# Optimization experiments

Hardware: AMD Instinct MI355X
Metric: run time of the kernel (lower is better)

The kernel has to match this reference:

```python
import jax, jax.numpy as jnp
import numpy as np

N_NODES = 50000
N_EDGES = 1600000
IN_FEAT = 48
OUT_FEAT = 48
NUM_RELS = 8


def setup_inputs() -> dict:
    key = jax.random.key(0)
    ks = jax.random.split(key, 9)
    # xavier-ish scale for relu gain
    s1 = float(np.sqrt(2.0) * np.sqrt(6.0 / (IN_FEAT + IN_FEAT)))
    s2 = float(np.sqrt(2.0) * np.sqrt(6.0 / (IN_FEAT + OUT_FEAT)))
    return {
        "inputs": jax.random.normal(ks[0], (N_NODES, IN_FEAT), dtype=jnp.float32),
        "norm": jax.random.uniform(ks[1], (N_EDGES, 1), dtype=jnp.float32),
        "weight1": jax.random.uniform(ks[2], (NUM_RELS, IN_FEAT, IN_FEAT), jnp.float32, -s1, s1),
        "weight2": jax.random.uniform(ks[3], (NUM_RELS, IN_FEAT, OUT_FEAT), jnp.float32, -s2, s2),
        "bias1": jax.random.normal(ks[4], (IN_FEAT,), dtype=jnp.float32) * 0.1,
        "bias2": jax.random.normal(ks[5], (OUT_FEAT,), dtype=jnp.float32) * 0.1,
        "src": jax.random.randint(ks[6], (N_EDGES,), 0, N_NODES, dtype=jnp.int64) if jax.config.jax_enable_x64 else jax.random.randint(ks[6], (N_EDGES,), 0, N_NODES).astype(jnp.int32),
        "dst": jax.random.randint(ks[7], (N_EDGES,), 0, N_NODES).astype(jnp.int32),
        "rel_type": jax.random.randint(ks[8], (N_EDGES,), 0, NUM_RELS).astype(jnp.int32),
    }


def reference(inputs, norm, weight1, weight2, bias1, bias2, src, dst, rel_type):
    # Message depends only on (src node, relation): precompute per (node, rel).
    # Stage 1: h1[n,r,:] = relu(h[n] @ W1[r] + b1)   -> [N, R, in]
    h1 = jax.nn.relu(jnp.einsum('ni,rij->nrj', inputs, weight1) + bias1)
    # Stage 2: h2[n,r,:] = h1[n,r] @ W2[r]           -> [N, R, out]
    h2 = jnp.einsum('nrj,rjo->nro', h1, weight2)
    # Per-edge gather + norm scaling                 -> [E, out]
    msg = h2[src, rel_type] * norm
    # Scatter-sum aggregation to destination nodes   -> [N, out]
    agg = jax.ops.segment_sum(msg, dst, num_segments=inputs.shape[0])
    # apply_func: bias2 + activation
    return jax.nn.relu(agg + bias2)
```

## Files before the change

### kernel.cpp

```cpp
#include <hip/hip_runtime.h>

#define NN 50000
#define EE 1600000
#define FF 48
#define RR 8
#define H2_ROW 64
#define LSTR 72
#define CAP 96

#define XB 3125
#define WB 8
#define ZB 49
#define K1GRID (XB + WB + ZB)

#define H2TILES 391
#define H2BLKS (H2TILES * RR)
#define K2GRID (H2BLKS * 3)

typedef __attribute__((ext_vector_type(8))) short frag8;
typedef __attribute__((ext_vector_type(4))) float frag4f;

__device__ inline unsigned short bf16r(float f) {
    unsigned u = __float_as_uint(f);
    return (unsigned short)((u + 0x7FFFu + ((u >> 16) & 1u)) >> 16);
}
__device__ inline unsigned bf16pack2(float a, float b) {
    return (unsigned)bf16r(a) | ((unsigned)bf16r(b) << 16);
}

__global__ __launch_bounds__(256) void pre_kernel(
    const float* __restrict__ X, const float* __restrict__ W1,
    const float* __restrict__ W2, unsigned short* __restrict__ Xb,
    unsigned short* __restrict__ W1t, unsigned short* __restrict__ W2t,
    int* __restrict__ count)
{
    int b = blockIdx.x;
    if (b < XB) {
        int g = b * 256 + threadIdx.x;
        int seg = g & 15;
        uint2 v = make_uint2(0u, 0u);
        if (seg < 12) {
            float4 x = ((const float4*)X)[(size_t)(g >> 4) * 12 + seg];
            v = make_uint2(bf16pack2(x.x, x.y), bf16pack2(x.z, x.w));
        }
        ((uint2*)Xb)[g] = v;
        return;
    }
    if (b < XB + WB) {
        int r = b - XB;
        const float* w1 = W1 + (size_t)r * FF * FF;
        const float* w2 = W2 + (size_t)r * FF * FF;
        for (int idx = threadIdx.x; idx < 48 * 64; idx += 256) {
            int j = idx >> 6, k = idx & 63;
            W1t[(size_t)r * 48 * 64 + idx] = (k < FF) ? bf16r(w1[k * FF + j]) : (unsigned short)0;
            W2t[(size_t)r * 48 * 64 + idx] = (k < FF) ? bf16r(w2[k * FF + j]) : (unsigned short)0;
        }
        return;
    }
    int z = (b - XB - WB) * 256 + threadIdx.x;
    if (z < 12500) ((int4*)count)[z] = make_int4(0, 0, 0, 0);
}

__global__ __launch_bounds__(256) void h2_place_kernel(
    const unsigned short* __restrict__ Xb, const unsigned short* __restrict__ W1t,
    const unsigned short* __restrict__ W2t, const float* __restrict__ B1,
    const int* __restrict__ srcv, const int* __restrict__ dstv,
    const int* __restrict__ relv, const float* __restrict__ norm,
    int* __restrict__ count, unsigned* __restrict__ payload,
    unsigned short* __restrict__ H2)
{
    __shared__ unsigned short h1s[128 * LSTR];
    int b = blockIdx.x;
    int bmod = b - (b / 3) * 3;
    if (bmod != 0) {
        int p = (b / 3) * 2 + bmod - 1;
        int e = p * 256 + threadIdx.x;
        if (e < EE) {
            int d = dstv[e];
            int pos = atomicAdd(&count[d], 1);
            unsigned qn = (unsigned)(norm[e] * 8192.0f + 0.5f);
            if (qn > 8191u) qn = 8191u;
            unsigned rec = ((unsigned)(srcv[e] * 8 + relv[e]) << 13) | qn;
            if ((unsigned)pos < (unsigned)CAP)
                __builtin_nontemporal_store(rec, &payload[(size_t)d * CAP + pos]);
        }
        return;
    }
    int h    = b / 3;
    int r    = h & 7;
    int tile = h >> 3;
    int tid  = threadIdx.x;
    int w    = tid >> 6, ln = tid & 63, q = ln >> 4, lq = ln & 15;
    int nb   = tile * 128 + w * 32;

    unsigned short* myh1 = &h1s[(w * 32) * LSTR];
    for (int i = ln; i < 32 * 12; i += 64) {
        int rr = i / 12, cs = i - rr * 12;
        *(unsigned*)&myh1[rr * LSTR + 48 + cs * 2] = 0;
    }

    int row0 = nb + lq;      if (row0 >= NN) row0 = NN - 1;
    int row1 = nb + 16 + lq; if (row1 >= NN) row1 = NN - 1;
    const frag8 a00 = *(const frag8*)&Xb[(size_t)row0 * 64 + q * 8];
    const frag8 a01 = *(const frag8*)&Xb[(size_t)row0 * 64 + 32 + q * 8];
    const frag8 a10 = *(const frag8*)&Xb[(size_t)row1 * 64 + q * 8];
    const frag8 a11 = *(const frag8*)&Xb[(size_t)row1 * 64 + 32 + q * 8];

    const unsigned short* w1r = W1t + (size_t)r * 48 * 64;
    const unsigned short* w2r = W2t + (size_t)r * 48 * 64;

    #pragma unroll
    for (int t = 0; t < 3; ++t) {
        int col = t * 16 + lq;
        frag8 b0 = *(const frag8*)&w1r[(col << 6) + q * 8];
        frag8 b1 = *(const frag8*)&w1r[(col << 6) + 32 + q * 8];
        float bc = B1[col];
        frag4f acc0 = {bc, bc, bc, bc};
        frag4f acc1 = {bc, bc, bc, bc};
        acc0 = __builtin_amdgcn_mfma_f32_16x16x32_bf16(a00, b0, acc0, 0, 0, 0);
        acc0 = __builtin_amdgcn_mfma_f32_16x16x32_bf16(a01, b1, acc0, 0, 0, 0);
        acc1 = __builtin_amdgcn_mfma_f32_16x16x32_bf16(a10, b0, acc1, 0, 0, 0);
        acc1 = __builtin_amdgcn_mfma_f32_16x16x32_bf16(a11, b1, acc1, 0, 0, 0);
        #pragma unroll
        for (int g = 0; g < 4; ++g) {
            myh1[(q * 4 + g) * LSTR + col]      = bf16r(fmaxf(acc0[g], 0.0f));
            myh1[(16 + q * 4 + g) * LSTR + col] = bf16r(fmaxf(acc1[g], 0.0f));
        }
    }

    const frag8 c00 = *(const frag8*)&myh1[lq * LSTR + q * 8];
    const frag8 c01 = *(const frag8*)&myh1[lq * LSTR + 32 + q * 8];
    const frag8 c10 = *(const frag8*)&myh1[(16 + lq) * LSTR + q * 8];
    const frag8 c11 = *(const frag8*)&myh1[(16 + lq) * LSTR + 32 + q * 8];

    #pragma unroll
    for (int t = 0; t < 3; ++t) {
        int col = t * 16 + lq;
        frag8 b0 = *(const frag8*)&w2r[(col << 6) + q * 8];
        frag8 b1 = *(const frag8*)&w2r[(col << 6) + 32 + q * 8];
        frag4f acc0 = {0.f, 0.f, 0.f, 0.f};
        frag4f acc1 = {0.f, 0.f, 0.f, 0.f};
        acc0 = __builtin_amdgcn_mfma_f32_16x16x32_bf16(c00, b0, acc0, 0, 0, 0);
        acc0 = __builtin_amdgcn_mfma_f32_16x16x32_bf16(c01, b1, acc0, 0, 0, 0);
        acc1 = __builtin_amdgcn_mfma_f32_16x16x32_bf16(c10, b0, acc1, 0, 0, 0);
        acc1 = __builtin_amdgcn_mfma_f32_16x16x32_bf16(c11, b1, acc1, 0, 0, 0);
        #pragma unroll
        for (int g = 0; g < 4; ++g) {
            int n0 = nb + q * 4 + g;
            int n1 = nb + 16 + q * 4 + g;
            if (n0 < NN) H2[((size_t)n0 * RR + r) * H2_ROW + col] = bf16r(acc0[g]);
            if (n1 < NN) H2[((size_t)n1 * RR + r) * H2_ROW + col] = bf16r(acc1[g]);
        }
    }
}

__global__ __launch_bounds__(256) void gather_kernel(
    const unsigned short* __restrict__ H2, const unsigned* __restrict__ payload,
    const int* __restrict__ count, const float* __restrict__ B2,
    float* __restrict__ out)
{
    unsigned tid = blockIdx.x * 256u + threadIdx.x;
    unsigned n = tid / 12u;
    unsigned c = tid - n * 12u;
    if (n >= NN) return;

    int cnt = count[n];
    if (cnt > CAP) cnt = CAP;
    if (cnt < 0) cnt = 0;
    const unsigned* pl = payload + (size_t)n * CAP;
    float a0 = 0.f, a1 = 0.f, a2 = 0.f, a3 = 0.f;

    int e = 0;
    for (; e + 8 <= cnt; e += 8) {
        unsigned p[8];
        #pragma unroll
        for (int k = 0; k < 8; ++k) p[k] = pl[e + k];
        uint2 v[8];
        #pragma unroll
        for (int k = 0; k < 8; ++k)
            v[k] = ((const uint2*)(H2 + (size_t)(p[k] >> 13) * H2_ROW))[c];
        #pragma unroll
        for (int k = 0; k < 8; ++k) {
            float nm = (float)(p[k] & 8191u) * (1.0f / 8192.0f);
            a0 = fmaf(__uint_as_float(v[k].x << 16),         nm, a0);
            a1 = fmaf(__uint_as_float(v[k].x & 0xFFFF0000u), nm, a1);
            a2 = fmaf(__uint_as_float(v[k].y << 16),         nm, a2);
            a3 = fmaf(__uint_as_float(v[k].y & 0xFFFF0000u), nm, a3);
        }
    }
    for (; e < cnt; ++e) {
        unsigned p = pl[e];
        float nm = (float)(p & 8191u) * (1.0f / 8192.0f);
        uint2 v = ((const uint2*)(H2 + (size_t)(p >> 13) * H2_ROW))[c];
        a0 = fmaf(__uint_as_float(v.x << 16),         nm, a0);
        a1 = fmaf(__uint_as_float(v.x & 0xFFFF0000u), nm, a1);
        a2 = fmaf(__uint_as_float(v.y << 16),         nm, a2);
        a3 = fmaf(__uint_as_float(v.y & 0xFFFF0000u), nm, a3);
    }
    float4 b = ((const float4*)B2)[c];
    ((float4*)out)[(size_t)n * 12u + c] = make_float4(
        fmaxf(a0 + b.x, 0.f), fmaxf(a1 + b.y, 0.f),
        fmaxf(a2 + b.z, 0.f), fmaxf(a3 + b.w, 0.f));
}

extern "C" void kernel_launch(void* const* d_in, const int* in_sizes, int n_in,
                              void* d_out, int out_size, void* d_ws, size_t ws_size,
                              hipStream_t stream) {
    const float* X   = (const float*)d_in[0];
    const float* nrm = (const float*)d_in[1];
    const float* W1  = (const float*)d_in[2];
    const float* W2  = (const float*)d_in[3];
    const float* B1  = (const float*)d_in[4];
    const float* B2  = (const float*)d_in[5];
    const int*   src = (const int*)d_in[6];
    const int*   dst = (const int*)d_in[7];
    const int*   rel = (const int*)d_in[8];
    float* out = (float*)d_out;

    unsigned short* H2      = (unsigned short*)d_ws;
    unsigned*       payload = (unsigned*)(H2 + (size_t)NN * RR * H2_ROW);
    unsigned short* Xb      = (unsigned short*)(payload + (size_t)NN * CAP);
    unsigned short* W1t     = Xb + (size_t)NN * 64;
    unsigned short* W2t     = W1t + RR * 48 * 64;
    int*            count   = (int*)(W2t + RR * 48 * 64);

    pre_kernel<<<K1GRID, 256, 0, stream>>>(X, W1, W2, Xb, W1t, W2t, count);

    h2_place_kernel<<<K2GRID, 256, 0, stream>>>(
        Xb, W1t, W2t, B1, src, dst, rel, nrm, count, payload, H2);

    unsigned total = (unsigned)NN * 12u;
    gather_kernel<<<(total + 255) / 256, 256, 0, stream>>>(
        H2, payload, count, B2, out);
}
```

Baseline: 230.0 us.

## Fuse input bf16 conversion into h2 kernel, memset counts, unroll gather by 16

```diff
diff --git a/kernel.cpp b/kernel.cpp
--- a/kernel.cpp
+++ b/kernel.cpp
@@ -8,10 +8,7 @@
 #define LSTR 72
 #define CAP 96
 
-#define XB 3125
 #define WB 8
-#define ZB 49
-#define K1GRID (XB + WB + ZB)
 
 #define H2TILES 391
 #define H2BLKS (H2TILES * RR)
@@ -27,42 +24,29 @@
 __device__ inline unsigned bf16pack2(float a, float b) {
     return (unsigned)bf16r(a) | ((unsigned)bf16r(b) << 16);
 }
+__device__ inline frag8 pack8(float4 a, float4 b) {
+    union { frag8 f; unsigned u[4]; } r;
+    r.u[0] = bf16pack2(a.x, a.y); r.u[1] = bf16pack2(a.z, a.w);
+    r.u[2] = bf16pack2(b.x, b.y); r.u[3] = bf16pack2(b.z, b.w);
+    return r.f;
+}
 
 __global__ __launch_bounds__(256) void pre_kernel(
-    const float* __restrict__ X, const float* __restrict__ W1,
-    const float* __restrict__ W2, unsigned short* __restrict__ Xb,
-    unsigned short* __restrict__ W1t, unsigned short* __restrict__ W2t,
-    int* __restrict__ count)
+    const float* __restrict__ W1, const float* __restrict__ W2,
+    unsigned short* __restrict__ W1t, unsigned short* __restrict__ W2t)
 {
-    int b = blockIdx.x;
-    if (b < XB) {
-        int g = b * 256 + threadIdx.x;
-        int seg = g & 15;
-        uint2 v = make_uint2(0u, 0u);
-        if (seg < 12) {
-            float4 x = ((const float4*)X)[(size_t)(g >> 4) * 12 + seg];
-            v = make_uint2(bf16pack2(x.x, x.y), bf16pack2(x.z, x.w));
-        }
-        ((uint2*)Xb)[g] = v;
-        return;
-    }
-    if (b < XB + WB) {
-        int r = b - XB;
-        const float* w1 = W1 + (size_t)r * FF * FF;
-        const float* w2 = W2 + (size_t)r * FF * FF;
-        for (int idx = threadIdx.x; idx < 48 * 64; idx += 256) {
-            int j = idx >> 6, k = idx & 63;
-            W1t[(size_t)r * 48 * 64 + idx] = (k < FF) ? bf16r(w1[k * FF + j]) : (unsigned short)0;
-            W2t[(size_t)r * 48 * 64 + idx] = (k < FF) ? bf16r(w2[k * FF + j]) : (unsigned short)0;
-        }
-        return;
-    }
-    int z = (b - XB - WB) * 256 + threadIdx.x;
-    if (z < 12500) ((int4*)count)[z] = make_int4(0, 0, 0, 0);
+    int r = blockIdx.x;
+    const float* w1 = W1 + (size_t)r * FF * FF;
+    const float* w2 = W2 + (size_t)r * FF * FF;
+    for (int idx = threadIdx.x; idx < 48 * 64; idx += 256) {
+        int j = idx >> 6, k = idx & 63;
+        W1t[(size_t)r * 48 * 64 + idx] = (k < FF) ? bf16r(w1[k * FF + j]) : (unsigned short)0;
+        W2t[(size_t)r * 48 * 64 + idx] = (k < FF) ? bf16r(w2[k * FF + j]) : (unsigned short)0;
+    }
 }
 
 __global__ __launch_bounds__(256) void h2_place_kernel(
-    const unsigned short* __restrict__ Xb, const unsigned short* __restrict__ W1t,
+    const float* __restrict__ X, const unsigned short* __restrict__ W1t,
     const unsigned short* __restrict__ W2t, const float* __restrict__ B1,
     const int* __restrict__ srcv, const int* __restrict__ dstv,
     const int* __restrict__ relv, const float* __restrict__ norm,
@@ -101,10 +85,17 @@
 
     int row0 = nb + lq;      if (row0 >= NN) row0 = NN - 1;
     int row1 = nb + 16 + lq; if (row1 >= NN) row1 = NN - 1;
-    const frag8 a00 = *(const frag8*)&Xb[(size_t)row0 * 64 + q * 8];
-    const frag8 a01 = *(const frag8*)&Xb[(size_t)row0 * 64 + 32 + q * 8];
-    const frag8 a10 = *(const frag8*)&Xb[(size_t)row1 * 64 + q * 8];
-    const frag8 a11 = *(const frag8*)&Xb[(size_t)row1 * 64 + 32 + q * 8];
+    const float* x0 = X + (size_t)row0 * FF;
+    const float* x1 = X + (size_t)row1 * FF;
+
+    frag8 a00 = pack8(*(const float4*)(x0 + q * 8), *(const float4*)(x0 + q * 8 + 4));
+    frag8 a10 = pack8(*(const float4*)(x1 + q * 8), *(const float4*)(x1 + q * 8 + 4));
+    frag8 a01 = {0, 0, 0, 0, 0, 0, 0, 0};
+    frag8 a11 = {0, 0, 0, 0, 0, 0, 0, 0};
+    if (q < 2) {
+        a01 = pack8(*(const float4*)(x0 + 32 + q * 8), *(const float4*)(x0 + 36 + q * 8));
+        a11 = pack8(*(const float4*)(x1 + 32 + q * 8), *(const float4*)(x1 + 36 + q * 8));
+    }
 
     const unsigned short* w1r = W1t + (size_t)r * 48 * 64;
     const unsigned short* w2r = W2t + (size_t)r * 48 * 64;
@@ -171,6 +162,23 @@
     float a0 = 0.f, a1 = 0.f, a2 = 0.f, a3 = 0.f;
 
     int e = 0;
+    for (; e + 16 <= cnt; e += 16) {
+        unsigned p[16];
+        #pragma unroll
+        for (int k = 0; k < 16; ++k) p[k] = pl[e + k];
+        uint2 v[16];
+        #pragma unroll
+        for (int k = 0; k < 16; ++k)
+            v[k] = ((const uint2*)(H2 + (size_t)(p[k] >> 13) * H2_ROW))[c];
+        #pragma unroll
+        for (int k = 0; k < 16; ++k) {
+            float nm = (float)(p[k] & 8191u) * (1.0f / 8192.0f);
+            a0 = fmaf(__uint_as_float(v[k].x << 16),         nm, a0);
+            a1 = fmaf(__uint_as_float(v[k].x & 0xFFFF0000u), nm, a1);
+            a2 = fmaf(__uint_as_float(v[k].y << 16),         nm, a2);
+            a3 = fmaf(__uint_as_float(v[k].y & 0xFFFF0000u), nm, a3);
+        }
+    }
     for (; e + 8 <= cnt; e += 8) {
         unsigned p[8];
         #pragma unroll
@@ -219,15 +227,16 @@
 
     unsigned short* H2      = (unsigned short*)d_ws;
     unsigned*       payload = (unsigned*)(H2 + (size_t)NN * RR * H2_ROW);
-    unsigned short* Xb      = (unsigned short*)(payload + (size_t)NN * CAP);
-    unsigned short* W1t     = Xb + (size_t)NN * 64;
+    unsigned short* W1t     = (unsigned short*)(payload + (size_t)NN * CAP);
     unsigned short* W2t     = W1t + RR * 48 * 64;
     int*            count   = (int*)(W2t + RR * 48 * 64);
 
-    pre_kernel<<<K1GRID, 256, 0, stream>>>(X, W1, W2, Xb, W1t, W2t, count);
+    hipMemsetAsync(count, 0, (size_t)NN * sizeof(int), stream);
+
+    pre_kernel<<<WB, 256, 0, stream>>>(W1, W2, W1t, W2t);
 
     h2_place_kernel<<<K2GRID, 256, 0, stream>>>(
-        Xb, W1t, W2t, B1, src, dst, rel, nrm, count, payload, H2);
+        X, W1t, W2t, B1, src, dst, rel, nrm, count, payload, H2);
 
     unsigned total = (unsigned)NN * 12u;
     gather_kernel<<<(total + 255) / 256, 256, 0, stream>>>(
```

Measured after the change: 228.3 us. About the same (-0.7%).
